# Performance work log

Hardware: AMD Instinct MI355X
Metric: run time of the kernel (lower is better)

The kernel has to match this reference:

```python
import jax, jax.numpy as jnp
import numpy as np

N_EMBD = 1024
HEAD_SIZE = N_EMBD  # source bug: Block passes n_embd as head_size
EPS = 1e-5

def layernorm(x, g, b):
    mu = jnp.mean(x, axis=-1, keepdims=True)
    var = jnp.var(x, axis=-1, keepdims=True)
    return (x - mu) * jax.lax.rsqrt(var + EPS) * g + b

def setup_inputs() -> dict:
    key = jax.random.key(0)
    ks = jax.random.split(key, 8)
    B, T, C = 4, 2048, N_EMBD
    s = lambda fan_in: 1.0 / np.sqrt(fan_in)
    return {
        "x": jax.random.normal(ks[0], (B, T, C), dtype=jnp.float32),
        "Wk": jax.random.uniform(ks[1], (C, HEAD_SIZE), jnp.float32, -s(C), s(C)),
        "Wq": jax.random.uniform(ks[2], (C, HEAD_SIZE), jnp.float32, -s(C), s(C)),
        "Wv": jax.random.uniform(ks[3], (C, HEAD_SIZE), jnp.float32, -s(C), s(C)),
        "W1": jax.random.uniform(ks[4], (C, 4 * C), jnp.float32, -s(C), s(C)),
        "b1": jnp.zeros((4 * C,), jnp.float32),
        "W2": jax.random.uniform(ks[5], (4 * C, C), jnp.float32, -s(4 * C), s(4 * C)),
        "b2": jnp.zeros((C,), jnp.float32),
        "g1": jnp.ones((C,), jnp.float32),
        "be1": jnp.zeros((C,), jnp.float32),
        "g2": jnp.ones((C,), jnp.float32),
        "be2": jnp.zeros((C,), jnp.float32),
    }

def reference(x, Wk, Wq, Wv, W1, b1, W2, b2, g1, be1, g2, be2):
    B, T, C = x.shape
    h = layernorm(x, g1, be1)
    q = h @ Wq              # [B,T,H]
    k = h @ Wk
    v = h @ Wv
    wei = jnp.einsum('bth,bsh->bts', q, k) / jnp.sqrt(jnp.float32(C))
    causal = jnp.tril(jnp.ones((T, T), dtype=bool))
    wei = jnp.where(causal, wei, -jnp.inf)
    wei = jax.nn.softmax(wei, axis=-1)
    sa = jnp.einsum('bts,bsh->bth', wei, v)
    x = x + sa
    h2 = layernorm(x, g2, be2)
    ff = jax.nn.relu(h2 @ W1 + b1) @ W2 + b2
    return x + ff
```

## Files before the change

kernel.cpp:

```cpp
#include <hip/hip_runtime.h>
#include <hip/hip_bf16.h>


typedef __bf16 bf16x8_t __attribute__((ext_vector_type(8)));
typedef float f32x4_t __attribute__((ext_vector_type(4)));

__device__ __forceinline__ unsigned short f2bf(float f) {
    unsigned int u = __float_as_uint(f);
    u += 0x7fffu + ((u >> 16) & 1u);
    return (unsigned short)(u >> 16);
}
__device__ __forceinline__ float bf2f(unsigned short u) {
    return __uint_as_float((unsigned int)u << 16);
}

__device__ __forceinline__ void gload16(const void* g, void* lds) {
    __builtin_amdgcn_global_load_lds(
        (const __attribute__((address_space(1))) unsigned int*)g,
        (__attribute__((address_space(3))) unsigned int*)lds, 16, 0, 0);
}

#define SB0() __builtin_amdgcn_sched_barrier(0)
#define BAR() asm volatile("s_barrier" ::: "memory")
#define VM4_BAR() asm volatile("s_waitcnt vmcnt(4)\ns_barrier" ::: "memory")
#define VM0_BAR() asm volatile("s_waitcnt vmcnt(0)\ns_barrier" ::: "memory")

enum { EPI_F32 = 0, EPI_BF16 = 1, EPI_BIAS_RELU_BF16 = 2, EPI_RESID_F32 = 3,
       EPI_BIAS_RESID_F32 = 4 };

template <int EPI, bool CSKIP, bool KLIM>
__global__ __launch_bounds__(512, 2) void gemm256(
    const unsigned short* __restrict__ A,
    const unsigned short* __restrict__ Bm,
    void* __restrict__ Cout,
    const float* __restrict__ bias,
    const float* __restrict__ resid,
    int M, int N, int K, int lda, int ldb, float scale,
    long long batA, long long batB, long long batC, long long batR)
{
    __shared__ __align__(16) unsigned char lds[131072];

    const int gx = gridDim.x;
    const int nwg = gx * gridDim.y;
    int bl = blockIdx.y * gx + blockIdx.x;
    bl = (bl & 7) * (nwg >> 3) + (bl >> 3);
    const int bx = bl % gx, by = bl / gx;

    const int row0 = by * 256, col0 = bx * 256;
    if (CSKIP && col0 > row0) return;

    const int bz = blockIdx.z;
    const unsigned short* Ab = A + (long long)bz * batA + (long long)row0 * lda;
    const unsigned short* Bb = Bm + (long long)bz * batB + (long long)col0 * ldb;

    const int tid = threadIdx.x, lane = tid & 63, wid = tid >> 6;
    const int wrM = (wid >> 2) * 128;
    const int wcN = (wid & 3) * 64;
    const int lr = lane & 15, lg = lane >> 4;

    int Keff = K;
    if (KLIM) { int kl = row0 + 256; Keff = kl < K ? kl : K; }
    const int nkt = Keff >> 6;

    const int c0 = wid * 128 + lane;
    const int crow = c0 >> 2;
    const int sg = (c0 & 3) ^ ((c0 >> 3) & 3);
    const unsigned short* gA0 = Ab + (long long)crow * lda + sg * 8;
    const unsigned short* gA1 = gA0 + 16ll * lda;
    const unsigned short* gB0 = Bb + (long long)crow * ldb + sg * 8;
    const unsigned short* gB1 = gB0 + 16ll * ldb;

    const int sw = (lg ^ ((lr >> 1) & 3)) << 4;
    const int aoff = (wrM + lr) * 64 + sw;
    const int boff = 16384 + (wcN + lr) * 64 + sw;

    f32x4_t acc[8][4];
#pragma unroll
    for (int m = 0; m < 8; ++m)
#pragma unroll
        for (int n = 0; n < 4; ++n)
            acc[m][n] = (f32x4_t){0.f, 0.f, 0.f, 0.f};

    auto stage2 = [&](int b, int kk, int ktn) {
        const int ke = ktn * 64 + kk * 32;
        unsigned char* uA = lds + b * 65536 + kk * 32768 + wid * 2048;
        unsigned char* uB = uA + 16384;
        gload16(gA0 + ke, uA);
        gload16(gA1 + ke, uA + 1024);
        gload16(gB0 + ke, uB);
        gload16(gB1 + ke, uB + 1024);
    };

    bf16x8_t af[8], bv[4];
    auto dsAB = [&](int b, int kk) {
        const unsigned char* u = lds + b * 65536 + kk * 32768;
#pragma unroll
        for (int m = 0; m < 8; ++m)
            af[m] = *(const bf16x8_t*)(u + aoff + m * 1024);
#pragma unroll
        for (int n = 0; n < 4; ++n)
            bv[n] = *(const bf16x8_t*)(u + boff + n * 1024);
    };
    auto mf32 = [&]() {
        __builtin_amdgcn_s_setprio(1);
#pragma unroll
        for (int m = 0; m < 8; ++m)
#pragma unroll
            for (int n = 0; n < 4; ++n)
                acc[m][n] = __builtin_amdgcn_mfma_f32_16x16x32_bf16(
                    af[m], bv[n], acc[m][n], 0, 0, 0);
        __builtin_amdgcn_s_setprio(0);
    };

    stage2(0, 0, 0); stage2(0, 1, 0);
    VM4_BAR();

    int kt = 0;
    for (; kt < nkt - 1; ++kt) {
        const int buf = kt & 1, nb = buf ^ 1;
        dsAB(buf, 0);
        stage2(nb, 0, kt + 1);
        BAR(); SB0();
        mf32(); SB0();
        VM4_BAR();
        dsAB(buf, 1);
        stage2(nb, 1, kt + 1);
        BAR(); SB0();
        mf32(); SB0();
        VM4_BAR();
    }
    {
        const int buf = kt & 1;
        dsAB(buf, 0);
        BAR(); SB0();
        mf32(); SB0();
        VM0_BAR();
        dsAB(buf, 1);
        BAR(); SB0();
        mf32(); SB0();
    }

    const int ldc = N;
    float* Cf = (float*)Cout + (long long)bz * batC;
    unsigned short* Cb = (unsigned short*)Cout + (long long)bz * batC;
    const float* R = nullptr;
    if constexpr (EPI == EPI_RESID_F32 || EPI == EPI_BIAS_RESID_F32)
        R = resid + (long long)bz * batR;

#pragma unroll
    for (int m = 0; m < 8; ++m)
#pragma unroll
        for (int n = 0; n < 4; ++n)
#pragma unroll
            for (int j = 0; j < 4; ++j) {
                const int row = row0 + wrM + m * 16 + lg * 4 + j;
                const int col = col0 + wcN + n * 16 + lr;
                const long long idx = (long long)row * ldc + col;
                float v = acc[m][n][j] * scale;
                if constexpr (EPI == EPI_F32) {
                    Cf[idx] = v;
                } else if constexpr (EPI == EPI_BF16) {
                    Cb[idx] = f2bf(v);
                } else if constexpr (EPI == EPI_BIAS_RELU_BF16) {
                    v += bias[col];
                    v = v > 0.f ? v : 0.f;
                    Cb[idx] = f2bf(v);
                } else if constexpr (EPI == EPI_RESID_F32) {
                    Cf[idx] = v + R[idx];
                } else {
                    Cf[idx] = v + bias[col] + R[idx];
                }
            }
}

__global__ __launch_bounds__(256) void tconv_k(
    const float* __restrict__ in, unsigned short* __restrict__ out,
    int R, int Cc)
{
    __shared__ float t[64][65];
    const int r0 = blockIdx.y * 64, c0 = blockIdx.x * 64;
    const int tid = threadIdx.x;
    const int a = tid >> 4;
    const int b = tid & 15;
#pragma unroll
    for (int i = 0; i < 4; ++i) {
        const int row = a + i * 16;
        float4 v = *(const float4*)(in + (long long)(r0 + row) * Cc + c0 + b * 4);
        t[row][b * 4 + 0] = v.x; t[row][b * 4 + 1] = v.y;
        t[row][b * 4 + 2] = v.z; t[row][b * 4 + 3] = v.w;
    }
    __syncthreads();
#pragma unroll
    for (int i = 0; i < 4; ++i) {
        const int oc = a + i * 16;
        ushort4 o;
        o.x = f2bf(t[b * 4 + 0][oc]);
        o.y = f2bf(t[b * 4 + 1][oc]);
        o.z = f2bf(t[b * 4 + 2][oc]);
        o.w = f2bf(t[b * 4 + 3][oc]);
        *(ushort4*)(out + (long long)(c0 + oc) * R + r0 + b * 4) = o;
    }
}

__global__ __launch_bounds__(256) void vtrans_k(
    const unsigned short* __restrict__ in, unsigned short* __restrict__ out)
{
    __shared__ unsigned short t[64][72];
    const int r0 = blockIdx.x * 64;
    const int c0 = blockIdx.y * 64;
    const int tid = threadIdx.x;
#pragma unroll
    for (int i = 0; i < 2; ++i) {
        const int ch = tid * 2 + i;
        const int row = ch >> 3, cs = ch & 7;
        int4 v = *(const int4*)(in + (long long)(r0 + row) * 3072 + 2048 + c0 + cs * 8);
        *(int4*)&t[row][cs * 8] = v;
    }
    __syncthreads();
#pragma unroll
    for (int i = 0; i < 2; ++i) {
        const int w = tid * 2 + i;
        const int oc = w >> 3, orc = w & 7;
        unsigned short tmp[8];
#pragma unroll
        for (int j = 0; j < 8; ++j) tmp[j] = t[orc * 8 + j][oc];
        *(int4*)(out + (long long)(c0 + oc) * 8192 + r0 + orc * 8) = *(const int4*)tmp;
    }
}

__global__ __launch_bounds__(256) void ln_k(
    const float* __restrict__ x, const float* __restrict__ g,
    const float* __restrict__ be, unsigned short* __restrict__ out)
{
    const int wv = threadIdx.x >> 6, lane = threadIdx.x & 63;
    const long long row = blockIdx.x * 4 + wv;
    const float* xr = x + row * 1024;
    float4 v[4];
    float s = 0.f, q = 0.f;
#pragma unroll
    for (int j = 0; j < 4; ++j) {
        v[j] = *(const float4*)(xr + j * 256 + lane * 4);
        s += v[j].x + v[j].y + v[j].z + v[j].w;
        q += v[j].x * v[j].x + v[j].y * v[j].y + v[j].z * v[j].z + v[j].w * v[j].w;
    }
#pragma unroll
    for (int off = 32; off > 0; off >>= 1) {
        s += __shfl_xor(s, off);
        q += __shfl_xor(q, off);
    }
    const float mean = s * (1.0f / 1024.0f);
    const float var  = q * (1.0f / 1024.0f) - mean * mean;
    const float rstd = rsqrtf(var + 1e-5f);
#pragma unroll
    for (int j = 0; j < 4; ++j) {
        float4 gv = *(const float4*)(g + j * 256 + lane * 4);
        float4 bv = *(const float4*)(be + j * 256 + lane * 4);
        ushort4 o;
        o.x = f2bf((v[j].x - mean) * rstd * gv.x + bv.x);
        o.y = f2bf((v[j].y - mean) * rstd * gv.y + bv.y);
        o.z = f2bf((v[j].z - mean) * rstd * gv.z + bv.z);
        o.w = f2bf((v[j].w - mean) * rstd * gv.w + bv.w);
        *(ushort4*)(out + row * 1024 + j * 256 + lane * 4) = o;
    }
}

__global__ __launch_bounds__(256) void softmax_k(
    const unsigned short* __restrict__ S, unsigned short* __restrict__ P, int T)
{
    __shared__ float rowl[2048];
    __shared__ float sred[4];
    const int t = blockIdx.x;
    const long long base = ((long long)blockIdx.y * T + t) * (long long)T;
    const unsigned short* srow = S + base;
    unsigned short* prow = P + base;
    const int n = t + 1;
    const int lim = ((t >> 8) + 1) << 8;
    const int tid = threadIdx.x;

    const int n8 = n >> 3;
    for (int i = tid; i < n8; i += 256) {
        int4 r = ((const int4*)srow)[i];
        const unsigned short* u = (const unsigned short*)&r;
#pragma unroll
        for (int j = 0; j < 8; ++j) rowl[i * 8 + j] = bf2f(u[j]);
    }
    for (int i = (n8 << 3) + tid; i < n; i += 256) rowl[i] = bf2f(srow[i]);
    __syncthreads();

    float mx = -3.0e38f;
    for (int i = tid; i < n; i += 256) mx = fmaxf(mx, rowl[i]);
#pragma unroll
    for (int off = 32; off > 0; off >>= 1) mx = fmaxf(mx, __shfl_xor(mx, off));
    if ((tid & 63) == 0) sred[tid >> 6] = mx;
    __syncthreads();
    mx = fmaxf(fmaxf(sred[0], sred[1]), fmaxf(sred[2], sred[3]));
    __syncthreads();

    float sum = 0.f;
    for (int i = tid; i < n; i += 256) {
        float e = __expf(rowl[i] - mx);
        rowl[i] = e;
        sum += e;
    }
#pragma unroll
    for (int off = 32; off > 0; off >>= 1) sum += __shfl_xor(sum, off);
    if ((tid & 63) == 0) sred[tid >> 6] = sum;
    __syncthreads();
    sum = sred[0] + sred[1] + sred[2] + sred[3];
    const float inv = 1.0f / sum;

    for (int i = tid; i < n; i += 256) prow[i] = f2bf(rowl[i] * inv);
    for (int i = n + tid; i < lim; i += 256) prow[i] = 0;
}

__global__ __launch_bounds__(256) void ffadd_k(
    const float4* __restrict__ p0, const float4* __restrict__ p1,
    const float4* __restrict__ xr, const float4* __restrict__ b2,
    float4* __restrict__ out, int n4)
{
    int i = blockIdx.x * 256 + threadIdx.x;
    const int stride = gridDim.x * 256;
    for (; i < n4; i += stride) {
        float4 a = p0[i], b = p1[i], c = xr[i], d = b2[i & 255];
        float4 o;
        o.x = a.x + b.x + c.x + d.x;
        o.y = a.y + b.y + c.y + d.y;
        o.z = a.z + b.z + c.z + d.z;
        o.w = a.w + b.w + c.w + d.w;
        out[i] = o;
    }
}

extern "C" void kernel_launch(void* const* d_in, const int* in_sizes, int n_in,
                              void* d_out, int out_size, void* d_ws, size_t ws_size,
                              hipStream_t stream)
{
    const int B = 4, T = 2048, C = 1024, F = 4096;
    const float* x   = (const float*)d_in[0];
    const float* Wk  = (const float*)d_in[1];
    const float* Wq  = (const float*)d_in[2];
    const float* Wv  = (const float*)d_in[3];
    const float* W1  = (const float*)d_in[4];
    const float* b1  = (const float*)d_in[5];
    const float* W2  = (const float*)d_in[6];
    const float* b2  = (const float*)d_in[7];
    const float* g1  = (const float*)d_in[8];
    const float* be1 = (const float*)d_in[9];
    const float* g2  = (const float*)d_in[10];
    const float* be2 = (const float*)d_in[11];

    char* ws = (char*)d_ws;
    const size_t MB = 1ull << 20;
    unsigned short* h     = (unsigned short*)(ws + 0);
    unsigned short* qkv   = (unsigned short*)(ws + 16 * MB);
    unsigned short* vT    = (unsigned short*)(ws + 64 * MB);
    float*          pbuf  = (float*)(ws + 16 * MB);
    float*          xres  = (float*)(ws + 80 * MB);
    unsigned short* S     = (unsigned short*)(ws + 112 * MB);
    unsigned short* P     = (unsigned short*)(ws + 144 * MB);
    unsigned short* ff1   = (unsigned short*)(ws + 112 * MB);
    unsigned short* wqkvT = (unsigned short*)(ws + 176 * MB);
    unsigned short* w1T   = (unsigned short*)(ws + 182 * MB);
    unsigned short* w2T   = (unsigned short*)(ws + 190 * MB);

    tconv_k<<<dim3(16, 16), 256, 0, stream>>>(Wq, wqkvT, C, C);
    tconv_k<<<dim3(16, 16), 256, 0, stream>>>(Wk, wqkvT + C * C, C, C);
    tconv_k<<<dim3(16, 16), 256, 0, stream>>>(Wv, wqkvT + 2 * C * C, C, C);
    tconv_k<<<dim3(64, 16), 256, 0, stream>>>(W1, w1T, C, F);
    tconv_k<<<dim3(16, 64), 256, 0, stream>>>(W2, w2T, F, C);

    ln_k<<<dim3(B * T / 4), 256, 0, stream>>>(x, g1, be1, h);

    dim3 gqkv(3 * C / 256, (B * T) / 256, 1);
    gemm256<EPI_BF16, false, false><<<gqkv, 512, 0, stream>>>(
        h, wqkvT, qkv, nullptr, nullptr, B * T, 3 * C, C, C, C, 1.0f, 0, 0, 0, 0);

    vtrans_k<<<dim3(B * T / 64, C / 64), 256, 0, stream>>>(qkv, vT);

    dim3 gsc(T / 256, T / 256, B);
    gemm256<EPI_BF16, true, false><<<gsc, 512, 0, stream>>>(
        qkv, qkv + C, S, nullptr, nullptr, T, T, C, 3 * C, 3 * C, 0.03125f,
        (long long)T * 3 * C, (long long)T * 3 * C, (long long)T * T, 0);

    softmax_k<<<dim3(T, B), 256, 0, stream>>>(S, P, T);

    dim3 gsa(C / 256, T / 256, B);
    gemm256<EPI_RESID_F32, false, true><<<gsa, 512, 0, stream>>>(
        P, vT, xres, nullptr, x, T, C, T, T, B * T, 1.0f,
        (long long)T * T, (long long)T, (long long)T * C, (long long)T * C);

    ln_k<<<dim3(B * T / 4), 256, 0, stream>>>(xres, g2, be2, h);

    dim3 gf1(F / 256, (B * T) / 256, 1);
    gemm256<EPI_BIAS_RELU_BF16, false, false><<<gf1, 512, 0, stream>>>(
        h, w1T, ff1, b1, nullptr, B * T, F, C, C, C, 1.0f, 0, 0, 0, 0);

    dim3 gf2(C / 256, (B * T) / 256, 2);
    gemm256<EPI_F32, false, false><<<gf2, 512, 0, stream>>>(
        ff1, w2T, pbuf, nullptr, nullptr, B * T, C, F / 2, F, F, 1.0f,
        (long long)(F / 2), (long long)(F / 2), (long long)(B * T) * C, 0);

    ffadd_k<<<dim3(2048), 256, 0, stream>>>(
        (const float4*)pbuf, (const float4*)(pbuf + (long long)(B * T) * C),
        (const float4*)xres, (const float4*)b2, (float4*)d_out,
        (B * T) * C / 4);
}
```

Baseline: 390.8 us.

## Shrink GEMM tiles to 128x128 and fuse FF2 bias/residual epilogue

Switches the shared GEMM kernel from 256x256 tiles with 8 waves to 128x128 tiles with 4 waves and half the LDS. This raises the workgroup count and tightens causal skipping for the attention GEMMs; softmax zero-padding now follows the 128 granularity. The split-K FF2 GEMM with its separate reduction kernel is replaced by a single full-K GEMM whose epilogue adds bias and residual directly into the output. The barrier macro now also waits on lgkmcnt, and the smaller tiles lower arithmetic intensity per byte loaded from global memory.

New measurement: 381.0 us. 1.03x faster.

```diff
diff --git a/kernel.cpp b/kernel.cpp
--- a/kernel.cpp
+++ b/kernel.cpp
@@ -21,7 +21,7 @@
 }
 
 #define SB0() __builtin_amdgcn_sched_barrier(0)
-#define BAR() asm volatile("s_barrier" ::: "memory")
+#define BAR_LGKM() asm volatile("s_barrier\ns_waitcnt lgkmcnt(0)" ::: "memory")
 #define VM4_BAR() asm volatile("s_waitcnt vmcnt(4)\ns_barrier" ::: "memory")
 #define VM0_BAR() asm volatile("s_waitcnt vmcnt(0)\ns_barrier" ::: "memory")
 
@@ -29,7 +29,7 @@
        EPI_BIAS_RESID_F32 = 4 };
 
 template <int EPI, bool CSKIP, bool KLIM>
-__global__ __launch_bounds__(512, 2) void gemm256(
+__global__ __launch_bounds__(256, 2) void gemm128(
     const unsigned short* __restrict__ A,
     const unsigned short* __restrict__ Bm,
     void* __restrict__ Cout,
@@ -38,7 +38,7 @@
     int M, int N, int K, int lda, int ldb, float scale,
     long long batA, long long batB, long long batC, long long batR)
 {
-    __shared__ __align__(16) unsigned char lds[131072];
+    __shared__ __align__(16) unsigned char lds[65536];
 
     const int gx = gridDim.x;
     const int nwg = gx * gridDim.y;
@@ -46,7 +46,7 @@
     bl = (bl & 7) * (nwg >> 3) + (bl >> 3);
     const int bx = bl % gx, by = bl / gx;
 
-    const int row0 = by * 256, col0 = bx * 256;
+    const int row0 = by * 128, col0 = bx * 128;
     if (CSKIP && col0 > row0) return;
 
     const int bz = blockIdx.z;
@@ -54,12 +54,12 @@
     const unsigned short* Bb = Bm + (long long)bz * batB + (long long)col0 * ldb;
 
     const int tid = threadIdx.x, lane = tid & 63, wid = tid >> 6;
-    const int wrM = (wid >> 2) * 128;
-    const int wcN = (wid & 3) * 64;
+    const int wrM = (wid >> 1) * 64;
+    const int wcN = (wid & 1) * 64;
     const int lr = lane & 15, lg = lane >> 4;
 
     int Keff = K;
-    if (KLIM) { int kl = row0 + 256; Keff = kl < K ? kl : K; }
+    if (KLIM) { int kl = row0 + 128; Keff = kl < K ? kl : K; }
     const int nkt = Keff >> 6;
 
     const int c0 = wid * 128 + lane;
@@ -72,39 +72,39 @@
 
     const int sw = (lg ^ ((lr >> 1) & 3)) << 4;
     const int aoff = (wrM + lr) * 64 + sw;
-    const int boff = 16384 + (wcN + lr) * 64 + sw;
-
-    f32x4_t acc[8][4];
-#pragma unroll
-    for (int m = 0; m < 8; ++m)
+    const int boff = 8192 + (wcN + lr) * 64 + sw;
+
+    f32x4_t acc[4][4];
+#pragma unroll
+    for (int m = 0; m < 4; ++m)
 #pragma unroll
         for (int n = 0; n < 4; ++n)
             acc[m][n] = (f32x4_t){0.f, 0.f, 0.f, 0.f};
 
     auto stage2 = [&](int b, int kk, int ktn) {
         const int ke = ktn * 64 + kk * 32;
-        unsigned char* uA = lds + b * 65536 + kk * 32768 + wid * 2048;
-        unsigned char* uB = uA + 16384;
+        unsigned char* uA = lds + b * 32768 + kk * 16384 + wid * 2048;
+        unsigned char* uB = uA + 8192;
         gload16(gA0 + ke, uA);
         gload16(gA1 + ke, uA + 1024);
         gload16(gB0 + ke, uB);
         gload16(gB1 + ke, uB + 1024);
     };
 
-    bf16x8_t af[8], bv[4];
+    bf16x8_t af[4], bv[4];
     auto dsAB = [&](int b, int kk) {
-        const unsigned char* u = lds + b * 65536 + kk * 32768;
-#pragma unroll
-        for (int m = 0; m < 8; ++m)
+        const unsigned char* u = lds + b * 32768 + kk * 16384;
+#pragma unroll
+        for (int m = 0; m < 4; ++m)
             af[m] = *(const bf16x8_t*)(u + aoff + m * 1024);
 #pragma unroll
         for (int n = 0; n < 4; ++n)
             bv[n] = *(const bf16x8_t*)(u + boff + n * 1024);
     };
-    auto mf32 = [&]() {
+    auto mf16 = [&]() {
         __builtin_amdgcn_s_setprio(1);
 #pragma unroll
-        for (int m = 0; m < 8; ++m)
+        for (int m = 0; m < 4; ++m)
 #pragma unroll
             for (int n = 0; n < 4; ++n)
                 acc[m][n] = __builtin_amdgcn_mfma_f32_16x16x32_bf16(
@@ -120,24 +120,24 @@
         const int buf = kt & 1, nb = buf ^ 1;
         dsAB(buf, 0);
         stage2(nb, 0, kt + 1);
-        BAR(); SB0();
-        mf32(); SB0();
+        BAR_LGKM(); SB0();
+        mf16(); SB0();
         VM4_BAR();
         dsAB(buf, 1);
         stage2(nb, 1, kt + 1);
-        BAR(); SB0();
-        mf32(); SB0();
+        BAR_LGKM(); SB0();
+        mf16(); SB0();
         VM4_BAR();
     }
     {
         const int buf = kt & 1;
         dsAB(buf, 0);
-        BAR(); SB0();
-        mf32(); SB0();
+        BAR_LGKM(); SB0();
+        mf16(); SB0();
         VM0_BAR();
         dsAB(buf, 1);
-        BAR(); SB0();
-        mf32(); SB0();
+        BAR_LGKM(); SB0();
+        mf16(); SB0();
     }
 
     const int ldc = N;
@@ -148,7 +148,7 @@
         R = resid + (long long)bz * batR;
 
 #pragma unroll
-    for (int m = 0; m < 8; ++m)
+    for (int m = 0; m < 4; ++m)
 #pragma unroll
         for (int n = 0; n < 4; ++n)
 #pragma unroll
@@ -274,7 +274,7 @@
     const unsigned short* srow = S + base;
     unsigned short* prow = P + base;
     const int n = t + 1;
-    const int lim = ((t >> 8) + 1) << 8;
+    const int lim = ((t >> 7) + 1) << 7;
     const int tid = threadIdx.x;
 
     const int n8 = n >> 3;
@@ -311,24 +311,6 @@
 
     for (int i = tid; i < n; i += 256) prow[i] = f2bf(rowl[i] * inv);
     for (int i = n + tid; i < lim; i += 256) prow[i] = 0;
-}
-
-__global__ __launch_bounds__(256) void ffadd_k(
-    const float4* __restrict__ p0, const float4* __restrict__ p1,
-    const float4* __restrict__ xr, const float4* __restrict__ b2,
-    float4* __restrict__ out, int n4)
-{
-    int i = blockIdx.x * 256 + threadIdx.x;
-    const int stride = gridDim.x * 256;
-    for (; i < n4; i += stride) {
-        float4 a = p0[i], b = p1[i], c = xr[i], d = b2[i & 255];
-        float4 o;
-        o.x = a.x + b.x + c.x + d.x;
-        o.y = a.y + b.y + c.y + d.y;
-        o.z = a.z + b.z + c.z + d.z;
-        o.w = a.w + b.w + c.w + d.w;
-        out[i] = o;
-    }
 }
 
 extern "C" void kernel_launch(void* const* d_in, const int* in_sizes, int n_in,
@@ -354,7 +336,6 @@
     unsigned short* h     = (unsigned short*)(ws + 0);
     unsigned short* qkv   = (unsigned short*)(ws + 16 * MB);
     unsigned short* vT    = (unsigned short*)(ws + 64 * MB);
-    float*          pbuf  = (float*)(ws + 16 * MB);
     float*          xres  = (float*)(ws + 80 * MB);
     unsigned short* S     = (unsigned short*)(ws + 112 * MB);
     unsigned short* P     = (unsigned short*)(ws + 144 * MB);
@@ -371,37 +352,31 @@
 
     ln_k<<<dim3(B * T / 4), 256, 0, stream>>>(x, g1, be1, h);
 
-    dim3 gqkv(3 * C / 256, (B * T) / 256, 1);
-    gemm256<EPI_BF16, false, false><<<gqkv, 512, 0, stream>>>(
+    dim3 gqkv(3 * C / 128, (B * T) / 128, 1);
+    gemm128<EPI_BF16, false, false><<<gqkv, 256, 0, stream>>>(
         h, wqkvT, qkv, nullptr, nullptr, B * T, 3 * C, C, C, C, 1.0f, 0, 0, 0, 0);
 
     vtrans_k<<<dim3(B * T / 64, C / 64), 256, 0, stream>>>(qkv, vT);
 
-    dim3 gsc(T / 256, T / 256, B);
-    gemm256<EPI_BF16, true, false><<<gsc, 512, 0, stream>>>(
+    dim3 gsc(T / 128, T / 128, B);
+    gemm128<EPI_BF16, true, false><<<gsc, 256, 0, stream>>>(
         qkv, qkv + C, S, nullptr, nullptr, T, T, C, 3 * C, 3 * C, 0.03125f,
         (long long)T * 3 * C, (long long)T * 3 * C, (long long)T * T, 0);
 
     softmax_k<<<dim3(T, B), 256, 0, stream>>>(S, P, T);
 
-    dim3 gsa(C / 256, T / 256, B);
-    gemm256<EPI_RESID_F32, false, true><<<gsa, 512, 0, stream>>>(
+    dim3 gsa(C / 128, T / 128, B);
+    gemm128<EPI_RESID_F32, false, true><<<gsa, 256, 0, stream>>>(
         P, vT, xres, nullptr, x, T, C, T, T, B * T, 1.0f,
         (long long)T * T, (long long)T, (long long)T * C, (long long)T * C);
 
     ln_k<<<dim3(B * T / 4), 256, 0, stream>>>(xres, g2, be2, h);
 
-    dim3 gf1(F / 256, (B * T) / 256, 1);
-    gemm256<EPI_BIAS_RELU_BF16, false, false><<<gf1, 512, 0, stream>>>(
+    dim3 gf1(F / 128, (B * T) / 128, 1);
+    gemm128<EPI_BIAS_RELU_BF16, false, false><<<gf1, 256, 0, stream>>>(
         h, w1T, ff1, b1, nullptr, B * T, F, C, C, C, 1.0f, 0, 0, 0, 0);
 
-    dim3 gf2(C / 256, (B * T) / 256, 2);
-    gemm256<EPI_F32, false, false><<<gf2, 512, 0, stream>>>(
-        ff1, w2T, pbuf, nullptr, nullptr, B * T, C, F / 2, F, F, 1.0f,
-        (long long)(F / 2), (long long)(F / 2), (long long)(B * T) * C, 0);
-
-    ffadd_k<<<dim3(2048), 256, 0, stream>>>(
-        (const float4*)pbuf, (const float4*)(pbuf + (long long)(B * T) * C),
-        (const float4*)xres, (const float4*)b2, (float4*)d_out,
-        (B * T) * C / 4);
-}
+    dim3 gf2(C / 128, (B * T) / 128, 1);
+    gemm128<EPI_BIAS_RESID_F32, false, false><<<gf2, 256, 0, stream>>>(
+        ff1, w2T, (float*)d_out, b2, xres, B * T, C, F, F, F, 1.0f, 0, 0, 0, 0);
+}
```
